# Kernel optimization log

Hardware: AMD Instinct MI355X
Metric: run time of the kernel (lower is better)

Reference implementation:

```python
import jax, jax.numpy as jnp
import numpy as np

DIM = 1024
HEADS = 16
HEAD_DIM = DIM // HEADS
LAYERS = 8
HIDDEN = 4 * DIM
VOCAB = 266
MAX_POS = 32768
B = 4
L = 2048
SCALE = HEAD_DIM ** -0.5
EPS = 1e-5


def layer_norm(x, g, b):
    m = jnp.mean(x, axis=-1, keepdims=True)
    v = jnp.mean(jnp.square(x - m), axis=-1, keepdims=True)
    return (x - m) * jax.lax.rsqrt(v + EPS) * g + b


def setup_inputs() -> dict:
    key = jax.random.key(0)
    ks = jax.random.split(key, 16)
    s = 0.02
    return {
        "tokens": jax.random.randint(ks[0], (B, L), 0, VOCAB),
        "tok_emb": jax.random.normal(ks[1], (VOCAB, DIM), jnp.float32) * s,
        "pos_emb": jax.random.normal(ks[2], (MAX_POS, DIM), jnp.float32) * s,
        "ln1_g": jnp.ones((LAYERS, DIM), jnp.float32),
        "ln1_b": jnp.zeros((LAYERS, DIM), jnp.float32),
        "q_w": jax.random.normal(ks[3], (LAYERS, DIM, DIM), jnp.float32) * s,
        "k_w": jax.random.normal(ks[4], (LAYERS, DIM, DIM), jnp.float32) * s,
        "v_w": jax.random.normal(ks[5], (LAYERS, DIM, DIM), jnp.float32) * s,
        "o_w": jax.random.normal(ks[6], (LAYERS, DIM, DIM), jnp.float32) * s,
        "ln2_g": jnp.ones((LAYERS, DIM), jnp.float32),
        "ln2_b": jnp.zeros((LAYERS, DIM), jnp.float32),
        "w1_w": jax.random.normal(ks[7], (LAYERS, HIDDEN, DIM), jnp.float32) * s,
        "wg_w": jax.random.normal(ks[8], (LAYERS, HIDDEN, DIM), jnp.float32) * s,
        "w2_w": jax.random.normal(ks[9], (LAYERS, DIM, HIDDEN), jnp.float32) * s,
        "lnf_g": jnp.ones((DIM,), jnp.float32),
        "lnf_b": jnp.zeros((DIM,), jnp.float32),
        "lm_w": jax.random.normal(ks[10], (VOCAB, DIM), jnp.float32) * s,
    }


def reference(tokens, tok_emb, pos_emb, ln1_g, ln1_b, q_w, k_w, v_w, o_w,
              ln2_g, ln2_b, w1_w, wg_w, w2_w, lnf_g, lnf_b, lm_w):
    Bv, Lv = tokens.shape
    x = tok_emb[tokens] + pos_emb[jnp.arange(Lv)][None, :, :]  # [B,L,D]
    # strictly-upper-triangular causal mask (True = masked)
    rows = jnp.arange(Lv)
    mask = rows[None, :] > rows[:, None]  # [L,L], col > row
    pos_bias = jnp.arange(Lv, dtype=x.dtype) * 0.01  # [L]
    neg_inf = jnp.array(-jnp.inf, dtype=x.dtype)

    for i in range(LAYERS):
        h = layer_norm(x, ln1_g[i], ln1_b[i])
        q = jnp.einsum('bld,ed->ble', h, q_w[i]).reshape(Bv, Lv, HEADS, HEAD_DIM).transpose(0, 2, 1, 3)
        k = jnp.einsum('bld,ed->ble', h, k_w[i]).reshape(Bv, Lv, HEADS, HEAD_DIM).transpose(0, 2, 1, 3)
        v = jnp.einsum('bld,ed->ble', h, v_w[i]).reshape(Bv, Lv, HEADS, HEAD_DIM).transpose(0, 2, 1, 3)
        attn = jnp.einsum('bhqd,bhkd->bhqk', q, k) * SCALE
        attn = jnp.where(mask[None, None, :, :], neg_inf, attn)
        attn = attn + pos_bias[None, None, None, :]
        attn = jax.nn.softmax(attn, axis=-1)
        out = jnp.einsum('bhqk,bhkd->bhqd', attn, v).transpose(0, 2, 1, 3).reshape(Bv, Lv, DIM)
        attn_out = jnp.einsum('bld,ed->ble', out, o_w[i])
        x = x + attn_out
        h2 = layer_norm(x, ln2_g[i], ln2_b[i])
        ff = jnp.einsum('blh,dh->bld', jax.nn.silu(jnp.einsum('bld,hd->blh', h2, w1_w[i])) * jnp.einsum('bld,hd->blh', h2, wg_w[i]), w2_w[i])
        x = x + ff

    last = layer_norm(x[:, -1, :], lnf_g, lnf_b)  # [B, D]
    return jnp.einsum('bd,vd->bv', last, lm_w)  # [B, VOCAB]
```

## Files before the change

kernel.cpp:

```cpp
#include <hip/hip_runtime.h>
#include <hip/hip_bf16.h>
#include <math.h>

#define DIMD 1024
#define HEADS 16
#define HD 64
#define LAYERS 8
#define HIDDEN 4096
#define VOCAB 266
#define NB 4
#define SEQ 2048
#define ROWS (NB*SEQ)
#define LOG2E 1.4426950408889634f
#define QSCALE (0.125f * LOG2E)
#define BIAS2 (0.01f * LOG2E)
#define THR2 8.0f

typedef float f32x4 __attribute__((ext_vector_type(4)));
typedef __bf16 bf16x8 __attribute__((ext_vector_type(8)));
typedef __bf16 bf16x4 __attribute__((ext_vector_type(4)));

__device__ __forceinline__ f32x4 mfma16(bf16x8 a, bf16x8 b, f32x4 c) {
    return __builtin_amdgcn_mfma_f32_16x16x32_bf16(a, b, c, 0, 0, 0);
}

__device__ __forceinline__ void gload16(const __bf16* g, __bf16* l) {
    __builtin_amdgcn_global_load_lds(
        (const __attribute__((address_space(1))) void*)g,
        (__attribute__((address_space(3))) void*)l, 16, 0, 0);
}

__global__ void embed_kernel(const int* __restrict__ tok, const float* __restrict__ te,
                             const float* __restrict__ pe, float* __restrict__ x) {
    int row = blockIdx.x;
    int t = tok[row];
    int l = row & (SEQ - 1);
    int c = threadIdx.x;
    f32x4 tv = *(const f32x4*)(te + (size_t)t * DIMD + c * 4);
    f32x4 pv = *(const f32x4*)(pe + (size_t)l * DIMD + c * 4);
    *(f32x4*)(x + (size_t)row * DIMD + c * 4) = tv + pv;
}

__global__ void cvt_kernel(const float* q, const float* k, const float* v, const float* o,
                           const float* w1, const float* wg, const float* w2,
                           __bf16* __restrict__ dst) {
    const size_t MM = 1024 * 1024;
    const float* src; size_t n; size_t off; int ilv = 0;
    switch (blockIdx.y) {
        case 0: src = q;  n = MM;     off = 0;       break;
        case 1: src = k;  n = MM;     off = MM;      break;
        case 2: src = v;  n = MM;     off = 2 * MM;  break;
        case 3: src = o;  n = MM;     off = 3 * MM;  break;
        case 4: src = w1; n = 4 * MM; off = 4 * MM;  ilv = 1; break;
        case 5: src = wg; n = 4 * MM; off = 4 * MM;  ilv = 2; break;
        default: src = w2; n = 4 * MM; off = 12 * MM; break;
    }
    size_t stride = (size_t)gridDim.x * blockDim.x * 8;
    for (size_t i = ((size_t)blockIdx.x * blockDim.x + threadIdx.x) * 8; i < n; i += stride) {
        f32x4 a = *(const f32x4*)(src + i);
        f32x4 b = *(const f32x4*)(src + i + 4);
        bf16x8 ov;
        ov[0] = (__bf16)a[0]; ov[1] = (__bf16)a[1]; ov[2] = (__bf16)a[2]; ov[3] = (__bf16)a[3];
        ov[4] = (__bf16)b[0]; ov[5] = (__bf16)b[1]; ov[6] = (__bf16)b[2]; ov[7] = (__bf16)b[3];
        size_t di;
        if (ilv) {
            size_t row = i >> 10, col = i & 1023;
            di = off + (((row << 1) | (ilv - 1)) << 10) + col;
        } else {
            di = off + i;
        }
        *(bf16x8*)(dst + di) = ov;
    }
}

template<bool F32OUT>
__global__ void ln_kernel(const float* __restrict__ xin, size_t row_stride,
                          const float* __restrict__ g, const float* __restrict__ bb,
                          void* __restrict__ out) {
    int row = blockIdx.x;
    int c = threadIdx.x;
    const float* xr = xin + (size_t)row * row_stride;
    f32x4 v = *(const f32x4*)(xr + c * 4);
    float s = v[0] + v[1] + v[2] + v[3];
    float s2 = v[0]*v[0] + v[1]*v[1] + v[2]*v[2] + v[3]*v[3];
    #pragma unroll
    for (int o = 32; o; o >>= 1) { s += __shfl_xor(s, o); s2 += __shfl_xor(s2, o); }
    __shared__ float red[8];
    int w = c >> 6, lane = c & 63;
    if (lane == 0) { red[w] = s; red[4 + w] = s2; }
    __syncthreads();
    s = red[0] + red[1] + red[2] + red[3];
    s2 = red[4] + red[5] + red[6] + red[7];
    float mean = s * (1.f / DIMD);
    float var = s2 * (1.f / DIMD) - mean * mean;
    float rstd = rsqrtf(var + 1e-5f);
    f32x4 gv = *(const f32x4*)(g + c * 4);
    f32x4 bv = *(const f32x4*)(bb + c * 4);
    f32x4 o4;
    #pragma unroll
    for (int j = 0; j < 4; ++j) o4[j] = (v[j] - mean) * rstd * gv[j] + bv[j];
    if (F32OUT) {
        *(f32x4*)((float*)out + (size_t)row * DIMD + c * 4) = o4;
    } else {
        bf16x4 hv;
        #pragma unroll
        for (int j = 0; j < 4; ++j) hv[j] = (__bf16)o4[j];
        *(bf16x4*)((__bf16*)out + (size_t)row * DIMD + c * 4) = hv;
    }
}

template<int EPI>
__global__ __launch_bounds__(256, 2)
void gemm_bt(const __bf16* __restrict__ A, const __bf16* __restrict__ W,
             int M, int N, int K,
             __bf16* bdst, float* fdst, float scale) {
    __shared__ __bf16 As[128 * 64];
    __shared__ __bf16 Bs[128 * 64];
    int tid = threadIdx.x;
    int lane = tid & 63, w = tid >> 6;
    int wm = w >> 1, wn = w & 1;
    int g16 = lane >> 4, l16 = lane & 15;
    int m0 = blockIdx.y * 128, n0 = blockIdx.x * 128;
    f32x4 acc[4][4] = {};
    int trow = tid >> 3;
    int cs8 = ((tid & 7) ^ (trow & 7)) * 8;
    const __bf16* ga = A + (size_t)(m0 + trow) * K + cs8;
    const __bf16* gb = W + (size_t)(n0 + trow) * K + cs8;
    int xsw = (l16 & 7) << 4;

    for (int k0 = 0; k0 < K; k0 += 64) {
        #pragma unroll
        for (int p = 0; p < 4; ++p) {
            gload16(ga + (size_t)(p * 32) * K + k0, As + (p * 256 + w * 64) * 8);
            gload16(gb + (size_t)(p * 32) * K + k0, Bs + (p * 256 + w * 64) * 8);
        }
        __syncthreads();
        #pragma unroll
        for (int kk = 0; kk < 2; ++kk) {
            bf16x8 af[4], bfv[4];
            #pragma unroll
            for (int f = 0; f < 4; ++f) {
                int ar = wm * 64 + f * 16 + l16;
                int br = wn * 64 + f * 16 + l16;
                af[f]  = *(const bf16x8*)((const char*)As + ((ar * 128 + kk * 64 + g16 * 16) ^ xsw));
                bfv[f] = *(const bf16x8*)((const char*)Bs + ((br * 128 + kk * 64 + g16 * 16) ^ xsw));
            }
            #pragma unroll
            for (int fm = 0; fm < 4; ++fm)
                #pragma unroll
                for (int fn = 0; fn < 4; ++fn)
                    acc[fm][fn] = mfma16(af[fm], bfv[fn], acc[fm][fn]);
        }
        __syncthreads();
    }

    #pragma unroll
    for (int fm = 0; fm < 4; ++fm) {
        int rbase = m0 + wm * 64 + fm * 16 + g16 * 4;
        #pragma unroll
        for (int fn = 0; fn < 4; ++fn) {
            int col = n0 + wn * 64 + fn * 16 + l16;
            if (EPI == 2) {
                #pragma unroll
                for (int j = 0; j < 4; ++j) {
                    size_t idx = (size_t)(rbase + j) * N + col;
                    fdst[idx] += acc[fm][fn][j];
                }
            }
        }
    }
}

template<int EPI>
__global__ __launch_bounds__(512, 2)
void gemm_big(const __bf16* __restrict__ A, const __bf16* __restrict__ W,
              int M, int N, int K, __bf16* __restrict__ bdst, float scale) {
    __shared__ __bf16 As[2][256 * 64];
    __shared__ __bf16 Bs[2][256 * 64];
    int tid = threadIdx.x;
    int lane = tid & 63, wid = tid >> 6;
    int wm = wid >> 2, wn = wid & 3;
    int g16 = lane >> 4, l16 = lane & 15;
    int m0 = blockIdx.y * 256, n0 = blockIdx.x * 256;

    int sr = tid >> 3;
    int cs8 = ((tid & 7) ^ (sr & 7)) * 8;
    const __bf16* ga = A + (size_t)(m0 + sr) * K + cs8;
    const __bf16* gb = W + (size_t)(n0 + sr) * K + cs8;

    auto stage = [&](int buf, int kof) {
        #pragma unroll
        for (int p = 0; p < 4; ++p) {
            gload16(ga + (size_t)(p * 64) * K + kof, As[buf] + (p * 64 + sr) * 64 + (tid & 7) * 8);
            gload16(gb + (size_t)(p * 64) * K + kof, Bs[buf] + (p * 64 + sr) * 64 + (tid & 7) * 8);
        }
    };

    f32x4 acc[8][4] = {};
    int NT = K >> 6;
    stage(0, 0);
    stage(1, 64);
    int xsw = (l16 & 7) << 4;

    for (int t = 0; t < NT; ++t) {
        int cur = t & 1;
        if (t + 1 < NT) asm volatile("s_waitcnt vmcnt(8)" ::: "memory");
        else            asm volatile("s_waitcnt vmcnt(0)" ::: "memory");
        __builtin_amdgcn_s_barrier();
        __builtin_amdgcn_sched_barrier(0);
        const char* Ab = (const char*)As[cur];
        const char* Bb = (const char*)Bs[cur];
        bf16x8 bfr[4][2];
        #pragma unroll
        for (int q = 0; q < 4; ++q) {
            bf16x8 afr[2][2];
            #pragma unroll
            for (int dm = 0; dm < 2; ++dm)
                #pragma unroll
                for (int kk = 0; kk < 2; ++kk) {
                    int row = wm * 128 + (q * 2 + dm) * 16 + l16;
                    afr[dm][kk] = *(const bf16x8*)(Ab + ((row * 128 + kk * 64 + g16 * 16) ^ xsw));
                }
            if (q == 0) {
                #pragma unroll
                for (int n = 0; n < 4; ++n)
                    #pragma unroll
                    for (int kk = 0; kk < 2; ++kk) {
                        int row = wn * 64 + n * 16 + l16;
                        bfr[n][kk] = *(const bf16x8*)(Bb + ((row * 128 + kk * 64 + g16 * 16) ^ xsw));
                    }
            }
            asm volatile("s_waitcnt lgkmcnt(0)" ::: "memory");
            __builtin_amdgcn_sched_barrier(0);
            __builtin_amdgcn_s_setprio(1);
            #pragma unroll
            for (int dm = 0; dm < 2; ++dm)
                #pragma unroll
                for (int n = 0; n < 4; ++n)
                    #pragma unroll
                    for (int kk = 0; kk < 2; ++kk)
                        acc[q * 2 + dm][n] = mfma16(afr[dm][kk], bfr[n][kk], acc[q * 2 + dm][n]);
            __builtin_amdgcn_s_setprio(0);
            __builtin_amdgcn_sched_barrier(0);
        }
        asm volatile("s_waitcnt lgkmcnt(0)" ::: "memory");
        __builtin_amdgcn_s_barrier();
        if (t + 2 < NT) stage(cur, (t + 2) << 6);
    }

    #pragma unroll
    for (int m = 0; m < 8; ++m) {
        int rbase = m0 + wm * 128 + m * 16 + g16 * 4;
        #pragma unroll
        for (int n = 0; n < 4; ++n) {
            int col = n0 + wn * 64 + n * 16 + l16;
            if (EPI == 5) {
                int which = col >> 10;
                int c = col & 1023;
                int hh = c >> 6, d = c & 63;
                if (which == 2) {
                    int b = rbase >> 11, l = rbase & 2047;
                    __bf16* vp = bdst + 2 * (size_t)ROWS * DIMD;
                    bf16x4 hv;
                    #pragma unroll
                    for (int j = 0; j < 4; ++j) hv[j] = (__bf16)acc[m][n][j];
                    *(bf16x4*)(vp + ((size_t)(b * HEADS + hh) * HD + d) * SEQ + l) = hv;
                } else {
                    float sc = (which == 0) ? scale : 1.f;
                    __bf16* base = bdst + (size_t)which * ROWS * DIMD;
                    #pragma unroll
                    for (int j = 0; j < 4; ++j) {
                        int row = rbase + j;
                        int b = row >> 11, l = row & 2047;
                        base[(((size_t)(b * HEADS + hh) * SEQ + l) << 6) + d] =
                            (__bf16)(acc[m][n][j] * sc);
                    }
                }
            } else if (EPI == 6) {
                #pragma unroll
                for (int j = 0; j < 4; ++j) {
                    float own = acc[m][n][j];
                    float other = __shfl_xor(own, 1);
                    if (!(l16 & 1)) {
                        float si = own / (1.f + __expf(-own));
                        bdst[(size_t)(rbase + j) * (N >> 1) + (col >> 1)] = (__bf16)(si * other);
                    }
                }
            }
        }
    }
}

__global__ __launch_bounds__(256, 2)
void attn_kernel(const __bf16* __restrict__ qt, const __bf16* __restrict__ kt,
                 const __bf16* __restrict__ vt, __bf16* __restrict__ ao) {
    int lin = blockIdx.x;
    int bxm = lin >> 6;
    int g = lin & 63;
    int hh = g & 15, b = g >> 4;
    int tid = threadIdx.x, lane = tid & 63, w = tid >> 6;
    int g16 = lane >> 4, l16 = lane & 15;

    __shared__ __bf16 Ks[2][64 * 64];
    __shared__ __bf16 Vs[2][64 * 64];
    __shared__ __bf16 Ps[4 * 32 * 72];
    __bf16* Pw = Ps + w * (32 * 72);

    const __bf16* qbase = qt + (size_t)(b * HEADS + hh) * SEQ * HD;
    const __bf16* kbase = kt + (size_t)(b * HEADS + hh) * SEQ * HD;
    const __bf16* vbase = vt + (size_t)(b * HEADS + hh) * HD * SEQ;

    int rr = lane >> 3;
    int cs8 = ((lane & 7) ^ rr) * 8;

    for (int s = 0; s < 2; ++s) {
        int qtile = (s == 0) ? (15 - bxm) : bxm;
        int qb = qtile * 128;
        int nt = (qb >> 6) + 2;

        bf16x8 qf[2][2];
        #pragma unroll
        for (int rb = 0; rb < 2; ++rb)
            #pragma unroll
            for (int kk = 0; kk < 2; ++kk)
                qf[rb][kk] = *(const bf16x8*)(qbase + (size_t)(qb + w * 32 + rb * 16 + l16) * HD + kk * 32 + g16 * 8);

        f32x4 accO[2][4] = {};
        float mrow[2][4], lrow[2][4];
        #pragma unroll
        for (int rb = 0; rb < 2; ++rb)
            #pragma unroll
            for (int j = 0; j < 4; ++j) { mrow[rb][j] = -1e30f; lrow[rb][j] = 0.f; }

        #pragma unroll
        for (int p = 0; p < 2; ++p) {
            int rbse = p * 32 + w * 8;
            gload16(kbase + (size_t)(rbse + rr) * HD + cs8, Ks[0] + rbse * 64);
            gload16(vbase + (size_t)(rbse + rr) * SEQ + cs8, Vs[0] + rbse * 64);
        }
        __syncthreads();

        for (int t = 0; t < nt; ++t) {
            int cur = t & 1;
            int kv0 = t << 6;

            if (t + 1 < nt) {
                int kv1 = kv0 + 64;
                #pragma unroll
                for (int p = 0; p < 2; ++p) {
                    int rbse = p * 32 + w * 8;
                    gload16(kbase + (size_t)(kv1 + rbse + rr) * HD + cs8, Ks[cur ^ 1] + rbse * 64);
                    gload16(vbase + (size_t)(rbse + rr) * SEQ + kv1 + cs8, Vs[cur ^ 1] + rbse * 64);
                }
            }

            f32x4 sacc[2][4] = {};
            __builtin_amdgcn_s_setprio(1);
            #pragma unroll
            for (int kk = 0; kk < 2; ++kk) {
                bf16x8 kf[4];
                #pragma unroll
                for (int nk = 0; nk < 4; ++nk) {
                    int key = nk * 16 + l16;
                    int bo = (key * 128 + (kk * 32 + g16 * 8) * 2) ^ ((key & 7) << 4);
                    kf[nk] = *(const bf16x8*)((const char*)Ks[cur] + bo);
                }
                #pragma unroll
                for (int rb = 0; rb < 2; ++rb)
                    #pragma unroll
                    for (int nk = 0; nk < 4; ++nk)
                        sacc[rb][nk] = mfma16(qf[rb][kk], kf[nk], sacc[rb][nk]);
            }
            __builtin_amdgcn_s_setprio(0);

            float mx8[2][4];
            #pragma unroll
            for (int rb = 0; rb < 2; ++rb) {
                #pragma unroll
                for (int j = 0; j < 4; ++j) {
                    int qrow = qb + w * 32 + rb * 16 + g16 * 4 + j;
                    float mx = -1e30f;
                    #pragma unroll
                    for (int nk = 0; nk < 4; ++nk) {
                        int key = kv0 + nk * 16 + l16;
                        float sc = sacc[rb][nk][j];
                        sc = (key <= qrow) ? (sc + BIAS2 * (float)key) : -1e30f;
                        sacc[rb][nk][j] = sc;
                        mx = fmaxf(mx, sc);
                    }
                    mx = fmaxf(mx, __shfl_xor(mx, 1));
                    mx = fmaxf(mx, __shfl_xor(mx, 2));
                    mx = fmaxf(mx, __shfl_xor(mx, 4));
                    mx = fmaxf(mx, __shfl_xor(mx, 8));
                    mx8[rb][j] = mx;
                }
            }

            bool ok = true;
            #pragma unroll
            for (int rb = 0; rb < 2; ++rb)
                #pragma unroll
                for (int j = 0; j < 4; ++j)
                    ok &= (mx8[rb][j] <= mrow[rb][j] + THR2);
            if (!__all(ok)) {
                #pragma unroll
                for (int rb = 0; rb < 2; ++rb) {
                    #pragma unroll
                    for (int j = 0; j < 4; ++j) {
                        float mnew = fmaxf(mrow[rb][j], mx8[rb][j]);
                        float rs = exp2f(mrow[rb][j] - mnew);
                        mrow[rb][j] = mnew;
                        lrow[rb][j] *= rs;
                        #pragma unroll
                        for (int nd = 0; nd < 4; ++nd) accO[rb][nd][j] *= rs;
                    }
                }
            }

            #pragma unroll
            for (int rb = 0; rb < 2; ++rb) {
                #pragma unroll
                for (int j = 0; j < 4; ++j) {
                    float m = mrow[rb][j];
                    float ps = 0.f;
                    #pragma unroll
                    for (int nk = 0; nk < 4; ++nk) {
                        float pp = exp2f(sacc[rb][nk][j] - m);
                        ps += pp;
                        Pw[(rb * 16 + g16 * 4 + j) * 72 + nk * 16 + l16] = (__bf16)pp;
                    }
                    lrow[rb][j] += ps;
                }
            }

            __builtin_amdgcn_s_setprio(1);
            #pragma unroll
            for (int kk = 0; kk < 2; ++kk) {
                bf16x8 pf[2];
                #pragma unroll
                for (int rb = 0; rb < 2; ++rb)
                    pf[rb] = *(const bf16x8*)(Pw + (rb * 16 + l16) * 72 + kk * 32 + g16 * 8);
                #pragma unroll
                for (int nd = 0; nd < 4; ++nd) {
                    int d = nd * 16 + l16;
                    int bo = (d * 128 + (kk * 32 + g16 * 8) * 2) ^ ((d & 7) << 4);
                    bf16x8 vf = *(const bf16x8*)((const char*)Vs[cur] + bo);
                    #pragma unroll
                    for (int rb = 0; rb < 2; ++rb)
                        accO[rb][nd] = mfma16(pf[rb], vf, accO[rb][nd]);
                }
            }
            __builtin_amdgcn_s_setprio(0);
            __syncthreads();
        }

        #pragma unroll
        for (int rb = 0; rb < 2; ++rb) {
            #pragma unroll
            for (int j = 0; j < 4; ++j) {
                float l = lrow[rb][j];
                l += __shfl_xor(l, 1);
                l += __shfl_xor(l, 2);
                l += __shfl_xor(l, 4);
                l += __shfl_xor(l, 8);
                lrow[rb][j] = 1.f / l;
            }
        }
        #pragma unroll
        for (int rb = 0; rb < 2; ++rb)
            #pragma unroll
            for (int nd = 0; nd < 4; ++nd)
                #pragma unroll
                for (int j = 0; j < 4; ++j) {
                    int row = qb + w * 32 + rb * 16 + g16 * 4 + j;
                    float o = accO[rb][nd][j] * lrow[rb][j];
                    ao[(size_t)(b * SEQ + row) * DIMD + hh * HD + nd * 16 + l16] = (__bf16)o;
                }
    }
}

__global__ void lm_head(const float* __restrict__ last, const float* __restrict__ lw,
                        float* __restrict__ out) {
    int v = blockIdx.x;
    int c = threadIdx.x, lane = c & 63, w = c >> 6;
    f32x4 wv = *(const f32x4*)(lw + (size_t)v * DIMD + c * 4);
    float a[NB];
    #pragma unroll
    for (int b = 0; b < NB; ++b) {
        f32x4 xv = *(const f32x4*)(last + b * DIMD + c * 4);
        a[b] = wv[0]*xv[0] + wv[1]*xv[1] + wv[2]*xv[2] + wv[3]*xv[3];
    }
    #pragma unroll
    for (int o = 32; o; o >>= 1)
        #pragma unroll
        for (int b = 0; b < NB; ++b) a[b] += __shfl_xor(a[b], o);
    __shared__ float red[4][NB];
    if (lane == 0)
        #pragma unroll
        for (int b = 0; b < NB; ++b) red[w][b] = a[b];
    __syncthreads();
    if (c < NB) {
        float s = red[0][c] + red[1][c] + red[2][c] + red[3][c];
        out[c * VOCAB + v] = s;
    }
}

extern "C" void kernel_launch(void* const* d_in, const int* in_sizes, int n_in,
                              void* d_out, int out_size, void* d_ws, size_t ws_size,
                              hipStream_t stream) {
    const int*   tokens  = (const int*)d_in[0];
    const float* tok_emb = (const float*)d_in[1];
    const float* pos_emb = (const float*)d_in[2];
    const float* ln1_g   = (const float*)d_in[3];
    const float* ln1_b   = (const float*)d_in[4];
    const float* q_w     = (const float*)d_in[5];
    const float* k_w     = (const float*)d_in[6];
    const float* v_w     = (const float*)d_in[7];
    const float* o_w     = (const float*)d_in[8];
    const float* ln2_g   = (const float*)d_in[9];
    const float* ln2_b   = (const float*)d_in[10];
    const float* w1_w    = (const float*)d_in[11];
    const float* wg_w    = (const float*)d_in[12];
    const float* w2_w    = (const float*)d_in[13];
    const float* lnf_g   = (const float*)d_in[14];
    const float* lnf_b   = (const float*)d_in[15];
    const float* lm_w    = (const float*)d_in[16];

    const size_t MM = 1024 * 1024;
    char* p = (char*)d_ws;
    __bf16* wbf = (__bf16*)p;          p += 16 * MM * 2;
    float*  x   = (float*)p;           p += (size_t)ROWS * DIMD * 4;
    __bf16* h   = (__bf16*)p;          p += (size_t)ROWS * DIMD * 2;
    __bf16* qt  = (__bf16*)p;          p += (size_t)ROWS * DIMD * 2;
    __bf16* kt  = (__bf16*)p;          p += (size_t)ROWS * DIMD * 2;
    __bf16* vt  = (__bf16*)p;          p += (size_t)ROWS * DIMD * 2;
    __bf16* ao  = (__bf16*)p;          p += (size_t)ROWS * DIMD * 2;
    __bf16* abuf= (__bf16*)p;          p += (size_t)ROWS * HIDDEN * 2;
    float*  last= (float*)p;           p += NB * DIMD * 4;

    embed_kernel<<<ROWS, 256, 0, stream>>>(tokens, tok_emb, pos_emb, x);

    for (int i = 0; i < LAYERS; ++i) {
        cvt_kernel<<<dim3(256, 7), 256, 0, stream>>>(
            q_w + (size_t)i * MM, k_w + (size_t)i * MM, v_w + (size_t)i * MM, o_w + (size_t)i * MM,
            w1_w + (size_t)i * 4 * MM, wg_w + (size_t)i * 4 * MM, w2_w + (size_t)i * 4 * MM, wbf);
        __bf16* wqkv = wbf;
        __bf16* wo   = wbf + 3 * MM;
        __bf16* w1g  = wbf + 4 * MM;
        __bf16* w2   = wbf + 12 * MM;

        ln_kernel<false><<<ROWS, 256, 0, stream>>>(x, DIMD, ln1_g + i * DIMD, ln1_b + i * DIMD, h);

        gemm_big<5><<<dim3(12, 32), 512, 0, stream>>>(h, wqkv, ROWS, 3 * DIMD, DIMD, qt, QSCALE);

        attn_kernel<<<512, 256, 0, stream>>>(qt, kt, vt, ao);

        gemm_bt<2><<<dim3(8, 64), 256, 0, stream>>>(ao, wo, ROWS, DIMD, DIMD, nullptr, x, 1.f);

        ln_kernel<false><<<ROWS, 256, 0, stream>>>(x, DIMD, ln2_g + i * DIMD, ln2_b + i * DIMD, h);

        gemm_big<6><<<dim3(32, 32), 512, 0, stream>>>(h, w1g, ROWS, 2 * HIDDEN, DIMD, abuf, 1.f);

        gemm_bt<2><<<dim3(8, 64), 256, 0, stream>>>(abuf, w2, ROWS, DIMD, HIDDEN, nullptr, x, 1.f);
    }

    ln_kernel<true><<<NB, 256, 0, stream>>>(x + (size_t)(SEQ - 1) * DIMD, (size_t)SEQ * DIMD,
                                            lnf_g, lnf_b, last);
    lm_head<<<VOCAB, 256, 0, stream>>>(last, lm_w, (float*)d_out);
}
```

Baseline: 4.312 ms.

## Rewrite big GEMM as 8-phase pipeline with half-tile LDS staging

Replaces the double-buffered 256x256 GEMM main loop with an 8-phase schedule that splits each LDS buffer into 128-row halves. Global-to-LDS loads for individual halves are issued between MFMA phases, so memory traffic interleaves more finely with compute. Each phase adds barriers and relies on hand-placed vmcnt waits, which costs synchronisation and risks races if the counts are wrong. It also raises the launch-bounds occupancy hint on the smaller gemm_bt kernel from 2 to 3 blocks, which may push the compiler to use fewer registers and spill.

```diff
diff --git a/kernel.cpp b/kernel.cpp
--- a/kernel.cpp
+++ b/kernel.cpp
@@ -110,7 +110,7 @@
 }
 
 template<int EPI>
-__global__ __launch_bounds__(256, 2)
+__global__ __launch_bounds__(256, 3)
 void gemm_bt(const __bf16* __restrict__ A, const __bf16* __restrict__ W,
              int M, int N, int K,
              __bf16* bdst, float* fdst, float scale) {
@@ -173,80 +173,112 @@
 
 template<int EPI>
 __global__ __launch_bounds__(512, 2)
-void gemm_big(const __bf16* __restrict__ A, const __bf16* __restrict__ W,
+void gemm_8ph(const __bf16* __restrict__ A, const __bf16* __restrict__ W,
               int M, int N, int K, __bf16* __restrict__ bdst, float scale) {
-    __shared__ __bf16 As[2][256 * 64];
-    __shared__ __bf16 Bs[2][256 * 64];
+    __shared__ __bf16 As[2][2][128 * 64];
+    __shared__ __bf16 Bs[2][2][128 * 64];
     int tid = threadIdx.x;
     int lane = tid & 63, wid = tid >> 6;
     int wm = wid >> 2, wn = wid & 3;
     int g16 = lane >> 4, l16 = lane & 15;
     int m0 = blockIdx.y * 256, n0 = blockIdx.x * 256;
 
-    int sr = tid >> 3;
-    int cs8 = ((tid & 7) ^ (sr & 7)) * 8;
-    const __bf16* ga = A + (size_t)(m0 + sr) * K + cs8;
-    const __bf16* gb = W + (size_t)(n0 + sr) * K + cs8;
-
-    auto stage = [&](int buf, int kof) {
-        #pragma unroll
-        for (int p = 0; p < 4; ++p) {
-            gload16(ga + (size_t)(p * 64) * K + kof, As[buf] + (p * 64 + sr) * 64 + (tid & 7) * 8);
-            gload16(gb + (size_t)(p * 64) * K + kof, Bs[buf] + (p * 64 + sr) * 64 + (tid & 7) * 8);
-        }
+    int sr = tid >> 3, ch = tid & 7;
+    int cs8 = (ch ^ (sr & 7)) * 8;
+    int xsw = (l16 & 7) << 4;
+
+    const __bf16* gA = A + (size_t)(m0 + sr) * K + cs8;
+    const __bf16* gB = W + (size_t)(n0 + sr) * K + cs8;
+
+    auto stA = [&](int buf, int half, int kt) {
+        const __bf16* g = gA + (size_t)(half * 128) * K + kt * 64;
+        __bf16* l = &As[buf][half][sr * 64 + ch * 8];
+        gload16(g, l);
+        gload16(g + (size_t)64 * K, l + 64 * 64);
     };
+    auto stB = [&](int buf, int half, int kt) {
+        const __bf16* g = gB + (size_t)(half * 128) * K + kt * 64;
+        __bf16* l = &Bs[buf][half][sr * 64 + ch * 8];
+        gload16(g, l);
+        gload16(g + (size_t)64 * K, l + 64 * 64);
+    };
 
     f32x4 acc[8][4] = {};
-    int NT = K >> 6;
-    stage(0, 0);
-    stage(1, 64);
-    int xsw = (l16 & 7) << 4;
-
-    for (int t = 0; t < NT; ++t) {
-        int cur = t & 1;
-        if (t + 1 < NT) asm volatile("s_waitcnt vmcnt(8)" ::: "memory");
-        else            asm volatile("s_waitcnt vmcnt(0)" ::: "memory");
-        __builtin_amdgcn_s_barrier();
-        __builtin_amdgcn_sched_barrier(0);
-        const char* Ab = (const char*)As[cur];
-        const char* Bb = (const char*)Bs[cur];
-        bf16x8 bfr[4][2];
-        #pragma unroll
-        for (int q = 0; q < 4; ++q) {
-            bf16x8 afr[2][2];
-            #pragma unroll
-            for (int dm = 0; dm < 2; ++dm)
-                #pragma unroll
-                for (int kk = 0; kk < 2; ++kk) {
-                    int row = wm * 128 + (q * 2 + dm) * 16 + l16;
-                    afr[dm][kk] = *(const bf16x8*)(Ab + ((row * 128 + kk * 64 + g16 * 16) ^ xsw));
-                }
-            if (q == 0) {
-                #pragma unroll
-                for (int n = 0; n < 4; ++n)
-                    #pragma unroll
-                    for (int kk = 0; kk < 2; ++kk) {
-                        int row = wn * 64 + n * 16 + l16;
-                        bfr[n][kk] = *(const bf16x8*)(Bb + ((row * 128 + kk * 64 + g16 * 16) ^ xsw));
-                    }
-            }
-            asm volatile("s_waitcnt lgkmcnt(0)" ::: "memory");
-            __builtin_amdgcn_sched_barrier(0);
-            __builtin_amdgcn_s_setprio(1);
-            #pragma unroll
-            for (int dm = 0; dm < 2; ++dm)
-                #pragma unroll
-                for (int n = 0; n < 4; ++n)
-                    #pragma unroll
-                    for (int kk = 0; kk < 2; ++kk)
-                        acc[q * 2 + dm][n] = mfma16(afr[dm][kk], bfr[n][kk], acc[q * 2 + dm][n]);
-            __builtin_amdgcn_s_setprio(0);
-            __builtin_amdgcn_sched_barrier(0);
-        }
-        asm volatile("s_waitcnt lgkmcnt(0)" ::: "memory");
-        __builtin_amdgcn_s_barrier();
-        if (t + 2 < NT) stage(cur, (t + 2) << 6);
-    }
+    bf16x8 bfr[4][2];
+
+    auto dsA = [&](int buf, int q, bf16x8 (&afr)[2][2]) {
+        const char* base = (const char*)&As[buf][wm][0];
+        #pragma unroll
+        for (int dm = 0; dm < 2; ++dm)
+            #pragma unroll
+            for (int kk = 0; kk < 2; ++kk) {
+                int row = (q * 2 + dm) * 16 + l16;
+                afr[dm][kk] = *(const bf16x8*)(base + ((row * 128 + kk * 64 + g16 * 16) ^ xsw));
+            }
+    };
+    auto dsB = [&](int buf) {
+        const char* base = (const char*)&Bs[buf][wn >> 1][0];
+        #pragma unroll
+        for (int n = 0; n < 4; ++n)
+            #pragma unroll
+            for (int kk = 0; kk < 2; ++kk) {
+                int row = (wn & 1) * 64 + n * 16 + l16;
+                bfr[n][kk] = *(const bf16x8*)(base + ((row * 128 + kk * 64 + g16 * 16) ^ xsw));
+            }
+    };
+    auto mm = [&](int q, bf16x8 (&afr)[2][2]) {
+        #pragma unroll
+        for (int dm = 0; dm < 2; ++dm)
+            #pragma unroll
+            for (int n = 0; n < 4; ++n)
+                #pragma unroll
+                for (int kk = 0; kk < 2; ++kk)
+                    acc[q * 2 + dm][n] = mfma16(afr[dm][kk], bfr[n][kk], acc[q * 2 + dm][n]);
+    };
+
+#define PH_PRE                                               \
+    __builtin_amdgcn_sched_barrier(0);                       \
+    __builtin_amdgcn_s_barrier();                            \
+    asm volatile("s_waitcnt lgkmcnt(0)" ::: "memory");       \
+    __builtin_amdgcn_sched_barrier(0);                       \
+    __builtin_amdgcn_s_setprio(1);
+#define PH_POST                                              \
+    __builtin_amdgcn_s_setprio(0);                           \
+    __builtin_amdgcn_sched_barrier(0);                       \
+    __builtin_amdgcn_s_barrier();
+
+    int NI = K >> 7;
+
+    stA(0, 0, 0); stA(0, 1, 0); stB(0, 0, 0); stB(0, 1, 0);
+    stB(1, 0, 1); stB(1, 1, 1);
+    asm volatile("s_waitcnt vmcnt(4)" ::: "memory");
+    __builtin_amdgcn_s_barrier();
+
+    for (int it = 0; it < NI; ++it) {
+        bool more = (it + 1 < NI);
+        int t1 = 2 * it + 1, t2 = t1 + 1, t3 = t1 + 2;
+        { bf16x8 afr[2][2]; dsA(0, 0, afr); dsB(0); stA(1, 0, t1);
+          PH_PRE; mm(0, afr); PH_POST; }
+        { bf16x8 afr[2][2]; dsA(0, 1, afr); stA(1, 1, t1);
+          PH_PRE; mm(1, afr); PH_POST; }
+        { bf16x8 afr[2][2]; dsA(0, 2, afr); if (more) stB(0, 0, t2);
+          PH_PRE; mm(2, afr); PH_POST; }
+        { bf16x8 afr[2][2]; dsA(0, 3, afr); if (more) stB(0, 1, t2);
+          if (more) asm volatile("s_waitcnt vmcnt(4)" ::: "memory");
+          else      asm volatile("s_waitcnt vmcnt(0)" ::: "memory");
+          PH_PRE; mm(3, afr); PH_POST; }
+        { bf16x8 afr[2][2]; dsA(1, 0, afr); dsB(1); if (more) stA(0, 0, t2);
+          PH_PRE; mm(0, afr); PH_POST; }
+        { bf16x8 afr[2][2]; dsA(1, 1, afr); if (more) stA(0, 1, t2);
+          PH_PRE; mm(1, afr); PH_POST; }
+        { bf16x8 afr[2][2]; dsA(1, 2, afr); if (more) stB(1, 0, t3);
+          PH_PRE; mm(2, afr); PH_POST; }
+        { bf16x8 afr[2][2]; dsA(1, 3, afr); if (more) stB(1, 1, t3);
+          if (more) asm volatile("s_waitcnt vmcnt(4)" ::: "memory");
+          PH_PRE; mm(3, afr); PH_POST; }
+    }
+#undef PH_PRE
+#undef PH_POST
 
     #pragma unroll
     for (int m = 0; m < 8; ++m) {
@@ -551,7 +583,7 @@
 
         ln_kernel<false><<<ROWS, 256, 0, stream>>>(x, DIMD, ln1_g + i * DIMD, ln1_b + i * DIMD, h);
 
-        gemm_big<5><<<dim3(12, 32), 512, 0, stream>>>(h, wqkv, ROWS, 3 * DIMD, DIMD, qt, QSCALE);
+        gemm_8ph<5><<<dim3(12, 32), 512, 0, stream>>>(h, wqkv, ROWS, 3 * DIMD, DIMD, qt, QSCALE);
 
         attn_kernel<<<512, 256, 0, stream>>>(qt, kt, vt, ao);
 
@@ -559,7 +591,7 @@
 
         ln_kernel<false><<<ROWS, 256, 0, stream>>>(x, DIMD, ln2_g + i * DIMD, ln2_b + i * DIMD, h);
 
-        gemm_big<6><<<dim3(32, 32), 512, 0, stream>>>(h, w1g, ROWS, 2 * HIDDEN, DIMD, abuf, 1.f);
+        gemm_8ph<6><<<dim3(32, 32), 512, 0, stream>>>(h, w1g, ROWS, 2 * HIDDEN, DIMD, abuf, 1.f);
 
         gemm_bt<2><<<dim3(8, 64), 256, 0, stream>>>(abuf, w2, ROWS, DIMD, HIDDEN, nullptr, x, 1.f);
     }
```

After: 4.124 ms. 1.05x faster.
